# Performance work log

Hardware: AMD Instinct MI355X
Metric: run time of the kernel (lower is better)

## Reference

```python
import jax, jax.numpy as jnp
import numpy as np

N_NODES = 100000
N_EDGES = 1600000
HID = 64


def _gcn_conv(x, src, dst, W, b, n_nodes):
    """PyG GCNConv: add self-loops, symmetric deg normalization, linear transform.
    out_i = sum_{j in N(i) u {i}} deg_i^{-1/2} deg_j^{-1/2} (x_j W) + b
    """
    h = x @ W  # [N, out] small matmul
    loops = jnp.arange(n_nodes, dtype=src.dtype)
    s = jnp.concatenate([src, loops])  # sources (message senders)
    d = jnp.concatenate([dst, loops])  # targets (aggregation index)
    deg = jax.ops.segment_sum(jnp.ones_like(d, dtype=h.dtype), d, num_segments=n_nodes)
    dinv = jnp.where(deg > 0, jax.lax.rsqrt(deg), 0.0)
    coef = dinv[s] * dinv[d]  # [E+N]
    msg = h[s] * coef[:, None]  # gather + scale (memory-bound)
    out = jax.ops.segment_sum(msg, d, num_segments=n_nodes)  # scatter-add
    return out + b


def setup_inputs() -> dict:
    key = jax.random.key(0)
    ks = jax.random.split(key, 16)
    x = jax.random.normal(ks[0], (N_NODES, 4), dtype=jnp.float32)
    edge_index = jax.random.randint(ks[1], (2, N_EDGES), 0, N_NODES, dtype=jnp.int64)
    s = 0.1
    params = {
        'W1': jax.random.normal(ks[2], (4, HID), dtype=jnp.float32) * s,
        'b1': jnp.zeros((HID,), dtype=jnp.float32),
        'W2': jax.random.normal(ks[3], (HID, HID), dtype=jnp.float32) * s,
        'b2': jnp.zeros((HID,), dtype=jnp.float32),
        'W3': jax.random.normal(ks[4], (HID, HID), dtype=jnp.float32) * s,
        'b3': jnp.zeros((HID,), dtype=jnp.float32),
        'Wp': jax.random.normal(ks[5], (HID, HID), dtype=jnp.float32) * s,
        'bp': jnp.zeros((HID,), dtype=jnp.float32),
        'Wa': jax.random.normal(ks[6], (HID, 4), dtype=jnp.float32) * s,
        'ba': jnp.zeros((4,), dtype=jnp.float32),
        'Wm': jax.random.normal(ks[7], (HID, 2), dtype=jnp.float32) * s,
        'bm': jnp.zeros((2,), dtype=jnp.float32),
        'Wg': jax.random.normal(ks[8], (HID, 3), dtype=jnp.float32) * s,
        'bg': jnp.zeros((3,), dtype=jnp.float32),
        'Wt': jax.random.normal(ks[9], (HID, 10), dtype=jnp.float32) * s,
        'bt': jnp.zeros((10,), dtype=jnp.float32),
    }
    return {'x': x, 'edge_index': edge_index, 'node_index': 0, **params}


def reference(x, edge_index, node_index, W1, b1, W2, b2, W3, b3, Wp, bp, Wa, ba, Wm, bm, Wg, bg, Wt, bt):
    src, dst = edge_index[0], edge_index[1]
    n = x.shape[0]
    # dropout is identity in eval mode
    h = jax.nn.relu(_gcn_conv(x, src, dst, W1, b1, n))
    h = jax.nn.relu(_gcn_conv(h, src, dst, W2, b2, n))
    h = jax.nn.relu(_gcn_conv(h, src, dst, W3, b3, n))
    node = h[node_index]
    node = jax.nn.relu(node @ Wp + bp)
    return (node @ Wa + ba, node @ Wm + bm, node @ Wg + bg, node @ Wt + bt)
```

## Files before the change

kernel.cpp:

```cpp
#include <hip/hip_runtime.h>


#define HID  64
#define CAP1 2048
#define CAP2 512
#define RB1  128
#define RB2  128
#define CL3  2048
#define VE   8
#define TPB  256

__device__ __forceinline__ int detect64(const void* ei) {
  const unsigned* e32 = (const unsigned*)ei;
  int lane = threadIdx.x & 63;
  bool z = (e32[2 * lane + 1] == 0u);
  return (__ballot(z) == ~0ull) ? 1 : 0;
}

__device__ __forceinline__ int ld_src(const void* ei, int is64, long long e) {
  return is64 ? (int)((const unsigned*)ei)[e << 1] : ((const int*)ei)[e];
}

__device__ __forceinline__ int load_dsts(const void* ei, long long E, long long base,
                                         int is64, int d[VE]) {
  int n = (int)((E - base) < VE ? (E - base) : VE);
  if (is64) {
    const unsigned long long* p = (const unsigned long long*)ei + E + base;
    if (n == VE && (((E + base) & 1) == 0)) {
      const ulonglong2* q = (const ulonglong2*)p;
#pragma unroll
      for (int k = 0; k < VE / 2; ++k) {
        ulonglong2 v = q[k];
        d[2 * k] = (int)(unsigned)v.x; d[2 * k + 1] = (int)(unsigned)v.y;
      }
    } else {
      for (int k = 0; k < n; ++k) d[k] = (int)(unsigned)p[k];
    }
  } else {
    const int* p = (const int*)ei + E + base;
    if (n == VE && (((E + base) & 3) == 0)) {
      const int4* q = (const int4*)p;
#pragma unroll
      for (int k = 0; k < VE / 4; ++k) {
        int4 v = q[k];
        d[4 * k] = v.x; d[4 * k + 1] = v.y; d[4 * k + 2] = v.z; d[4 * k + 3] = v.w;
      }
    } else {
      for (int k = 0; k < n; ++k) d[k] = p[k];
    }
  }
  return n;
}

__device__ __forceinline__ int load_dsts32(const int* dst32, long long E,
                                           long long base, int d[VE]) {
  int n = (int)((E - base) < VE ? (E - base) : VE);
  if (n == VE) {
    int4 a = ((const int4*)(dst32 + base))[0];
    int4 b = ((const int4*)(dst32 + base))[1];
    d[0] = a.x; d[1] = a.y; d[2] = a.z; d[3] = a.w;
    d[4] = b.x; d[5] = b.y; d[6] = b.z; d[7] = b.w;
  } else {
    for (int k = 0; k < n; ++k) d[k] = dst32[base + k];
  }
  return n;
}

__global__ void k_scanF1(const void* ei, int E, const int* nidx_p, int* dst32,
                         int* slot2, int* node2, int* cnt2, int* l3, int* ec3) {
  int is64 = detect64(ei);
  int nidx = *nidx_p;
  if (blockIdx.x == 0 && threadIdx.x == 0) {
    if (atomicCAS(&slot2[nidx], -1, -2) == -1) {
      int p = atomicAdd(cnt2, 1) & (CAP2 - 1);
      slot2[nidx] = p; node2[p] = nidx;
    }
  }
  long long base = ((long long)blockIdx.x * TPB + threadIdx.x) * VE;
  if (base >= E) return;
  int d[VE];
  int n = load_dsts(ei, E, base, is64, d);
  if (n == VE) {
    ((int4*)(dst32 + base))[0] = make_int4(d[0], d[1], d[2], d[3]);
    ((int4*)(dst32 + base))[1] = make_int4(d[4], d[5], d[6], d[7]);
  } else {
    for (int k = 0; k < n; ++k) dst32[base + k] = d[k];
  }
  for (int k = 0; k < n; ++k) {
    if (d[k] == nidx) {
      int s = ld_src(ei, is64, base + k);
      if (atomicCAS(&slot2[s], -1, -2) == -1) {
        int p = atomicAdd(cnt2, 1) & (CAP2 - 1);
        slot2[s] = p; node2[p] = s;
      }
      int q = atomicAdd(ec3, 1);
      if (q < CL3) l3[q] = s;
    }
  }
}

__global__ void k_scanF2(const void* ei, int E, const int* dst32,
                         const int* slot2, const int* node2, const int* cnt2,
                         int* slot1, int* node1, int* need, int* cnt1,
                         int* rc2, int* bl2) {
  int rows2 = min(*cnt2, CAP2);
  for (int r = threadIdx.x; r < rows2; r += TPB) {
    int i = node2[r];
    need[i] = 1;
    if (atomicCAS(&slot1[i], -1, -2) == -1) {
      int p = atomicAdd(cnt1, 1) & (CAP1 - 1);
      slot1[i] = p; node1[p] = i;
    }
  }
  int is64 = detect64(ei);
  long long base = ((long long)blockIdx.x * TPB + threadIdx.x) * VE;
  if (base >= E) return;
  int d[VE];
  int n = load_dsts32(dst32, E, base, d);
  for (int k = 0; k < n; ++k) {
    int ad = slot2[d[k]];
    if (ad >= 0) {
      int s = ld_src(ei, is64, base + k);
      need[s] = 1;
      if (atomicCAS(&slot1[s], -1, -2) == -1) {
        int p = atomicAdd(cnt1, 1) & (CAP1 - 1);
        slot1[s] = p; node1[p] = s;
      }
      int q = atomicAdd(&rc2[ad], 1);
      if (q < RB2) bl2[ad * RB2 + q] = s;
    }
  }
}

__global__ void k_scanS(const void* ei, int E, const int* dst32,
                        const int* slot1, int* need, int* rc1, int* bl1) {
  int is64 = detect64(ei);
  long long base = ((long long)blockIdx.x * TPB + threadIdx.x) * VE;
  if (base >= E) return;
  int d[VE];
  int n = load_dsts32(dst32, E, base, d);
  for (int k = 0; k < n; ++k) {
    int ad = slot1[d[k]];
    if (ad >= 0) {
      int s = ld_src(ei, is64, base + k);
      need[s] = 1;
      int q = atomicAdd(&rc1[ad], 1);
      if (q < RB1) bl1[ad * RB1 + q] = s;
    }
  }
}

__global__ void k_scanDeg(int E, const int* dst32, const int* need, int* deg) {
  long long base = ((long long)blockIdx.x * TPB + threadIdx.x) * VE;
  if (base >= E) return;
  int d[VE];
  int n = load_dsts32(dst32, E, base, d);
  for (int k = 0; k < n; ++k)
    if (need[d[k]]) atomicAdd(&deg[d[k]], 1);
}

__global__ void k_l1(const float* __restrict__ x, const float* __restrict__ W1,
                     const float* __restrict__ b1, const int* __restrict__ deg,
                     const int* __restrict__ node1, const int* __restrict__ cnt1,
                     const int* __restrict__ rc1, const int* __restrict__ bl1,
                     float* __restrict__ h1c) {
  int w = blockIdx.x * 4 + (threadIdx.x >> 6);
  int lane = threadIdx.x & 63;
  int rows = min(*cnt1, CAP1);
  if (w >= rows) return;
  int i = node1[w];
  float di = 1.0f / sqrtf((float)(deg[i] + 1));
  int cnt = min(rc1[w], RB1);
  float ax = 0.f, ay = 0.f, az = 0.f, aw = 0.f;
  for (int j = lane; j < cnt; j += 64) {
    int s = bl1[w * RB1 + j];
    float c = (1.0f / sqrtf((float)(deg[s] + 1))) * di;
    float4 xv = ((const float4*)x)[s];
    ax += c * xv.x; ay += c * xv.y; az += c * xv.z; aw += c * xv.w;
  }
#pragma unroll
  for (int t = 1; t < 64; t <<= 1) {
    ax += __shfl_xor(ax, t); ay += __shfl_xor(ay, t);
    az += __shfl_xor(az, t); aw += __shfl_xor(aw, t);
  }
  float4 xi = ((const float4*)x)[i];
  float dd = di * di;
  ax += dd * xi.x; ay += dd * xi.y; az += dd * xi.z; aw += dd * xi.w;
  float v = ax * W1[lane] + ay * W1[64 + lane] + az * W1[128 + lane] +
            aw * W1[192 + lane] + b1[lane];
  h1c[w * HID + lane] = v > 0.f ? v : 0.f;
}

__global__ __launch_bounds__(TPB) void k_l2tail(
    const float* W2, const float* b2, const int* deg,
    const int* node2, const int* cnt2, const int* slot1,
    const int* rc2, const int* bl2, const float* h1c, float* h2c,
    const int* nidx_p, const int* slot2, const int* l3, const int* ec3,
    const float* W3, const float* b3, const float* Wp, const float* bp,
    const float* Wa, const float* ba, const float* Wm, const float* bm,
    const float* Wg, const float* bg, const float* Wt, const float* bt,
    float* out) {
  __shared__ float h2s[64][HID];
  __shared__ float smA[4][HID];
  __shared__ float g3[HID];
  __shared__ float h3v[HID];
  __shared__ float pj[HID];
  __shared__ int   ssl[64];
  __shared__ float scc[64];
  int tid = threadIdx.x, wv = tid >> 6, lane = tid & 63;
  int nidx = *nidx_p;
  int rows = min(*cnt2, CAP2);

  for (int w = wv; w < rows; w += 4) {
    int i = node2[w];
    float di = 1.0f / sqrtf((float)(deg[i] + 1));
    int cnt = min(rc2[w], RB2);
    float acc = 0.f;
    for (int j0 = 0; j0 < cnt; j0 += 64) {
      int nb = min(64, cnt - j0);
      int sl = 0; float c = 0.f;
      if (lane < nb) {
        int s = bl2[w * RB2 + j0 + lane];
        sl = slot1[s];
        c = (1.0f / sqrtf((float)(deg[s] + 1))) * di;
      }
      for (int j = 0; j < nb; ++j)
        acc += __shfl(c, j) * h1c[__shfl(sl, j) * HID + lane];
    }
    acc += di * di * h1c[slot1[i] * HID + lane];
    smA[wv][lane] = acc;
    float v = b2[lane];
#pragma unroll 16
    for (int k = 0; k < HID; ++k) v += smA[wv][k] * W2[k * HID + lane];
    v = v > 0.f ? v : 0.f;
    if (w < 64) h2s[w][lane] = v; else h2c[w * HID + lane] = v;
  }
  __syncthreads();

  float dn = 1.0f / sqrtf((float)(deg[nidx] + 1));
  int cnt = min(*ec3, CL3);
  float acc = 0.f;
  for (int j0 = 0; j0 < cnt; j0 += 64) {
    int nb = min(64, cnt - j0);
    if (tid < nb) {
      int s = l3[j0 + tid];
      ssl[tid] = slot2[s];
      scc[tid] = (1.0f / sqrtf((float)(deg[s] + 1))) * dn;
    }
    __syncthreads();
    for (int j = wv; j < nb; j += 4) {
      int r = ssl[j];
      float hv = (r < 64) ? h2s[r][lane] : h2c[r * HID + lane];
      acc += scc[j] * hv;
    }
    __syncthreads();
  }
  smA[wv][lane] = acc;
  __syncthreads();
  if (wv == 0) {
    int r = slot2[nidx];
    float hv = (r < 64) ? h2s[r][lane] : h2c[r * HID + lane];
    g3[lane] = smA[0][lane] + smA[1][lane] + smA[2][lane] + smA[3][lane] +
               dn * dn * hv;
  }
  __syncthreads();
  if (wv == 0) {
    float v = b3[lane];
#pragma unroll 16
    for (int k = 0; k < HID; ++k) v += g3[k] * W3[k * HID + lane];
    h3v[lane] = v > 0.f ? v : 0.f;
  }
  __syncthreads();
  if (wv == 0) {
    float v = bp[lane];
#pragma unroll 16
    for (int k = 0; k < HID; ++k) v += h3v[k] * Wp[k * HID + lane];
    pj[lane] = v > 0.f ? v : 0.f;
  }
  __syncthreads();
  if (tid < 4) {
    float o = ba[tid];
    for (int k = 0; k < HID; ++k) o += pj[k] * Wa[k * 4 + tid];
    out[tid] = o;
  } else if (tid < 6) {
    int c = tid - 4; float o = bm[c];
    for (int k = 0; k < HID; ++k) o += pj[k] * Wm[k * 2 + c];
    out[tid] = o;
  } else if (tid < 9) {
    int c = tid - 6; float o = bg[c];
    for (int k = 0; k < HID; ++k) o += pj[k] * Wg[k * 3 + c];
    out[tid] = o;
  } else if (tid < 19) {
    int c = tid - 9; float o = bt[c];
    for (int k = 0; k < HID; ++k) o += pj[k] * Wt[k * 10 + c];
    out[tid] = o;
  }
}

extern "C" void kernel_launch(void* const* d_in, const int* in_sizes, int n_in,
                              void* d_out, int out_size, void* d_ws, size_t ws_size,
                              hipStream_t stream) {
  const float* x  = (const float*)d_in[0];
  const void*  ei = d_in[1];
  const int* nidx = (const int*)d_in[2];
  const float* W1 = (const float*)d_in[3];
  const float* b1 = (const float*)d_in[4];
  const float* W2 = (const float*)d_in[5];
  const float* b2 = (const float*)d_in[6];
  const float* W3 = (const float*)d_in[7];
  const float* b3 = (const float*)d_in[8];
  const float* Wp = (const float*)d_in[9];
  const float* bp = (const float*)d_in[10];
  const float* Wa = (const float*)d_in[11];
  const float* ba = (const float*)d_in[12];
  const float* Wm = (const float*)d_in[13];
  const float* bm = (const float*)d_in[14];
  const float* Wg = (const float*)d_in[15];
  const float* bg = (const float*)d_in[16];
  const float* Wt = (const float*)d_in[17];
  const float* bt = (const float*)d_in[18];
  float* out = (float*)d_out;

  int N = in_sizes[0] / 4;
  int E = in_sizes[1] / 2;

  char* w = (char*)d_ws;
  size_t o = 0;
  auto take = [&](size_t bytes) -> void* {
    void* p = w + o;
    o += (bytes + 255) & ~(size_t)255;
    return p;
  };
  size_t zeroBytes = (size_t)(3 + 2 * N + CAP1 + CAP2) * 4;
  int* zr = (int*)take(zeroBytes);
  int* cnt1 = zr + 0;
  int* cnt2 = zr + 1;
  int* ec3  = zr + 2;
  int* deg  = zr + 3;
  int* need = deg + N;
  int* rc1  = need + N;
  int* rc2  = rc1 + CAP1;
  int* slots = (int*)take((size_t)2 * N * 4);
  int* slot1 = slots;
  int* slot2 = slots + N;
  int*   dst32 = (int*)take((size_t)E * 4);
  int*   node1 = (int*)take((size_t)CAP1 * 4);
  int*   node2 = (int*)take((size_t)CAP2 * 4);
  int*   bl1   = (int*)take((size_t)CAP1 * RB1 * 4);
  int*   bl2   = (int*)take((size_t)CAP2 * RB2 * 4);
  int*   l3    = (int*)take((size_t)CL3 * 4);
  float* h1c   = (float*)take((size_t)CAP1 * HID * 4);
  float* h2c   = (float*)take((size_t)CAP2 * HID * 4);

  int gS = (int)(((long long)E + TPB * VE - 1) / (TPB * VE));

  hipMemsetAsync(zr, 0x00, zeroBytes, stream);
  hipMemsetAsync(slots, 0xFF, (size_t)2 * N * 4, stream);
  k_scanF1 <<<gS, TPB, 0, stream>>>(ei, E, nidx, dst32, slot2, node2, cnt2, l3, ec3);
  k_scanF2 <<<gS, TPB, 0, stream>>>(ei, E, dst32, slot2, node2, cnt2,
                                    slot1, node1, need, cnt1, rc2, bl2);
  k_scanS  <<<gS, TPB, 0, stream>>>(ei, E, dst32, slot1, need, rc1, bl1);
  k_scanDeg<<<gS, TPB, 0, stream>>>(E, dst32, need, deg);
  k_l1     <<<CAP1 / 4, TPB, 0, stream>>>(x, W1, b1, deg, node1, cnt1, rc1, bl1, h1c);
  k_l2tail <<<1, TPB, 0, stream>>>(W2, b2, deg, node2, cnt2, slot1, rc2, bl2,
                                   h1c, h2c, nidx, slot2, l3, ec3, W3, b3,
                                   Wp, bp, Wa, ba, Wm, bm, Wg, bg, Wt, bt, out);
}
```

Measured before the change: 194.3 us.

## Split layer-2 aggregation out of single-block tail into a multi-block kernel

Layer-2 row computation previously ran inside a single 256-thread block, with four waves looping over up to 512 rows. It now runs as its own kernel with CAP2/4 blocks, one wave per row, and the tail kernel reads all h2 rows from global memory instead of partly from shared memory. This spreads the layer-2 gather and matvec across many CUs, at the cost of one extra kernel launch and the loss of the shared-memory cache for the first 64 rows.

```diff
diff --git a/kernel.cpp b/kernel.cpp
--- a/kernel.cpp
+++ b/kernel.cpp
@@ -191,52 +191,58 @@
   h1c[w * HID + lane] = v > 0.f ? v : 0.f;
 }
 
-__global__ __launch_bounds__(TPB) void k_l2tail(
-    const float* W2, const float* b2, const int* deg,
-    const int* node2, const int* cnt2, const int* slot1,
-    const int* rc2, const int* bl2, const float* h1c, float* h2c,
-    const int* nidx_p, const int* slot2, const int* l3, const int* ec3,
-    const float* W3, const float* b3, const float* Wp, const float* bp,
-    const float* Wa, const float* ba, const float* Wm, const float* bm,
-    const float* Wg, const float* bg, const float* Wt, const float* bt,
-    float* out) {
-  __shared__ float h2s[64][HID];
-  __shared__ float smA[4][HID];
+__global__ void k_l2(const float* __restrict__ W2, const float* __restrict__ b2,
+                     const int* __restrict__ deg, const int* __restrict__ node2,
+                     const int* __restrict__ cnt2, const int* __restrict__ slot1,
+                     const int* __restrict__ rc2, const int* __restrict__ bl2,
+                     const float* __restrict__ h1c, float* __restrict__ h2c) {
+  __shared__ float sh[4][HID];
+  int wv = threadIdx.x >> 6, lane = threadIdx.x & 63;
+  int w = blockIdx.x * 4 + wv;
+  int rows = min(*cnt2, CAP2);
+  if (w >= rows) return;
+  int i = node2[w];
+  float di = 1.0f / sqrtf((float)(deg[i] + 1));
+  int cnt = min(rc2[w], RB2);
+  float acc = 0.f;
+  for (int j0 = 0; j0 < cnt; j0 += 64) {
+    int nb = min(64, cnt - j0);
+    int sl = 0; float c = 0.f;
+    if (lane < nb) {
+      int s = bl2[w * RB2 + j0 + lane];
+      sl = slot1[s];
+      c = (1.0f / sqrtf((float)(deg[s] + 1))) * di;
+    }
+    for (int j = 0; j < nb; ++j) {
+      int slj = __shfl(sl, j);
+      float cj = __shfl(c, j);
+      acc += cj * h1c[slj * HID + lane];
+    }
+  }
+  acc += di * di * h1c[slot1[i] * HID + lane];
+  sh[wv][lane] = acc;
+  float v = b2[lane];
+#pragma unroll 16
+  for (int k = 0; k < HID; ++k) v += sh[wv][k] * W2[k * HID + lane];
+  h2c[w * HID + lane] = v > 0.f ? v : 0.f;
+}
+
+__global__ void k_tail(const int* nidx_p, const int* slot2, const int* deg,
+                       const float* h2c, const int* l3, const int* ec3,
+                       const float* W3, const float* b3,
+                       const float* Wp, const float* bp,
+                       const float* Wa, const float* ba,
+                       const float* Wm, const float* bm,
+                       const float* Wg, const float* bg,
+                       const float* Wt, const float* bt, float* out) {
+  __shared__ float part[4][HID];
   __shared__ float g3[HID];
-  __shared__ float h3v[HID];
-  __shared__ float pj[HID];
+  __shared__ float h3[HID];
+  __shared__ float p[HID];
   __shared__ int   ssl[64];
   __shared__ float scc[64];
   int tid = threadIdx.x, wv = tid >> 6, lane = tid & 63;
   int nidx = *nidx_p;
-  int rows = min(*cnt2, CAP2);
-
-  for (int w = wv; w < rows; w += 4) {
-    int i = node2[w];
-    float di = 1.0f / sqrtf((float)(deg[i] + 1));
-    int cnt = min(rc2[w], RB2);
-    float acc = 0.f;
-    for (int j0 = 0; j0 < cnt; j0 += 64) {
-      int nb = min(64, cnt - j0);
-      int sl = 0; float c = 0.f;
-      if (lane < nb) {
-        int s = bl2[w * RB2 + j0 + lane];
-        sl = slot1[s];
-        c = (1.0f / sqrtf((float)(deg[s] + 1))) * di;
-      }
-      for (int j = 0; j < nb; ++j)
-        acc += __shfl(c, j) * h1c[__shfl(sl, j) * HID + lane];
-    }
-    acc += di * di * h1c[slot1[i] * HID + lane];
-    smA[wv][lane] = acc;
-    float v = b2[lane];
-#pragma unroll 16
-    for (int k = 0; k < HID; ++k) v += smA[wv][k] * W2[k * HID + lane];
-    v = v > 0.f ? v : 0.f;
-    if (w < 64) h2s[w][lane] = v; else h2c[w * HID + lane] = v;
-  }
-  __syncthreads();
-
   float dn = 1.0f / sqrtf((float)(deg[nidx] + 1));
   int cnt = min(*ec3, CL3);
   float acc = 0.f;
@@ -248,51 +254,47 @@
       scc[tid] = (1.0f / sqrtf((float)(deg[s] + 1))) * dn;
     }
     __syncthreads();
-    for (int j = wv; j < nb; j += 4) {
-      int r = ssl[j];
-      float hv = (r < 64) ? h2s[r][lane] : h2c[r * HID + lane];
-      acc += scc[j] * hv;
-    }
+    for (int j = wv; j < nb; j += 4)
+      acc += scc[j] * h2c[ssl[j] * HID + lane];
     __syncthreads();
   }
-  smA[wv][lane] = acc;
+  part[wv][lane] = acc;
   __syncthreads();
   if (wv == 0) {
-    int r = slot2[nidx];
-    float hv = (r < 64) ? h2s[r][lane] : h2c[r * HID + lane];
-    g3[lane] = smA[0][lane] + smA[1][lane] + smA[2][lane] + smA[3][lane] +
-               dn * dn * hv;
+    float a = part[0][lane] + part[1][lane] + part[2][lane] + part[3][lane];
+    a += dn * dn * h2c[slot2[nidx] * HID + lane];
+    g3[lane] = a;
   }
   __syncthreads();
   if (wv == 0) {
     float v = b3[lane];
 #pragma unroll 16
     for (int k = 0; k < HID; ++k) v += g3[k] * W3[k * HID + lane];
-    h3v[lane] = v > 0.f ? v : 0.f;
+    h3[lane] = v > 0.f ? v : 0.f;
   }
   __syncthreads();
   if (wv == 0) {
-    float v = bp[lane];
+    float pv = bp[lane];
 #pragma unroll 16
-    for (int k = 0; k < HID; ++k) v += h3v[k] * Wp[k * HID + lane];
-    pj[lane] = v > 0.f ? v : 0.f;
+    for (int k = 0; k < HID; ++k) pv += h3[k] * Wp[k * HID + lane];
+    p[lane] = pv > 0.f ? pv : 0.f;
   }
   __syncthreads();
   if (tid < 4) {
     float o = ba[tid];
-    for (int k = 0; k < HID; ++k) o += pj[k] * Wa[k * 4 + tid];
+    for (int k = 0; k < HID; ++k) o += p[k] * Wa[k * 4 + tid];
     out[tid] = o;
   } else if (tid < 6) {
     int c = tid - 4; float o = bm[c];
-    for (int k = 0; k < HID; ++k) o += pj[k] * Wm[k * 2 + c];
+    for (int k = 0; k < HID; ++k) o += p[k] * Wm[k * 2 + c];
     out[tid] = o;
   } else if (tid < 9) {
     int c = tid - 6; float o = bg[c];
-    for (int k = 0; k < HID; ++k) o += pj[k] * Wg[k * 3 + c];
+    for (int k = 0; k < HID; ++k) o += p[k] * Wg[k * 3 + c];
     out[tid] = o;
   } else if (tid < 19) {
     int c = tid - 9; float o = bt[c];
-    for (int k = 0; k < HID; ++k) o += pj[k] * Wt[k * 10 + c];
+    for (int k = 0; k < HID; ++k) o += p[k] * Wt[k * 10 + c];
     out[tid] = o;
   }
 }
@@ -362,7 +364,7 @@
   k_scanS  <<<gS, TPB, 0, stream>>>(ei, E, dst32, slot1, need, rc1, bl1);
   k_scanDeg<<<gS, TPB, 0, stream>>>(E, dst32, need, deg);
   k_l1     <<<CAP1 / 4, TPB, 0, stream>>>(x, W1, b1, deg, node1, cnt1, rc1, bl1, h1c);
-  k_l2tail <<<1, TPB, 0, stream>>>(W2, b2, deg, node2, cnt2, slot1, rc2, bl2,
-                                   h1c, h2c, nidx, slot2, l3, ec3, W3, b3,
-                                   Wp, bp, Wa, ba, Wm, bm, Wg, bg, Wt, bt, out);
-}
+  k_l2     <<<CAP2 / 4, TPB, 0, stream>>>(W2, b2, deg, node2, cnt2, slot1, rc2, bl2, h1c, h2c);
+  k_tail   <<<1, TPB, 0, stream>>>(nidx, slot2, deg, h2c, l3, ec3, W3, b3, Wp, bp,
+                                   Wa, ba, Wm, bm, Wg, bg, Wt, bt, out);
+}
```

Result: faster. 172.6 us (-11.2%).

## Fuse degree scan, layer 1, layer 2 and tail into one persistent kernel

Applied to the files above, without the earlier changes.

Merges the degree-count scan, the layer-1 kernel, and the layer-2 plus tail kernel into one grid of 256 blocks. The stages are separated by atomic ticket counters with spin-waits, and late-arriving blocks carry on to the next stage while the others exit. Slot arrays now use 0 as the empty marker with values offset by one, so a single zeroing memset replaces the separate 0xFF memset. This removes kernel launch gaps and one memset, but relies on the waiting blocks being co-resident. It also drops the shared-memory cache of layer-2 rows and uses a fixed grid-stride for the degree scan.

```diff
diff --git a/kernel.cpp b/kernel.cpp
--- a/kernel.cpp
+++ b/kernel.cpp
@@ -9,6 +9,9 @@
 #define CL3  2048
 #define VE   8
 #define TPB  256
+#define GC   256
+#define NL1  128
+#define NL2  8
 
 __device__ __forceinline__ int detect64(const void* ei) {
   const unsigned* e32 = (const unsigned*)ei;
@@ -66,14 +69,15 @@
   return n;
 }
 
+
 __global__ void k_scanF1(const void* ei, int E, const int* nidx_p, int* dst32,
                          int* slot2, int* node2, int* cnt2, int* l3, int* ec3) {
   int is64 = detect64(ei);
   int nidx = *nidx_p;
   if (blockIdx.x == 0 && threadIdx.x == 0) {
-    if (atomicCAS(&slot2[nidx], -1, -2) == -1) {
+    if (atomicCAS(&slot2[nidx], 0, -1) == 0) {
       int p = atomicAdd(cnt2, 1) & (CAP2 - 1);
-      slot2[nidx] = p; node2[p] = nidx;
+      slot2[nidx] = p + 1; node2[p] = nidx;
     }
   }
   long long base = ((long long)blockIdx.x * TPB + threadIdx.x) * VE;
@@ -89,9 +93,9 @@
   for (int k = 0; k < n; ++k) {
     if (d[k] == nidx) {
       int s = ld_src(ei, is64, base + k);
-      if (atomicCAS(&slot2[s], -1, -2) == -1) {
+      if (atomicCAS(&slot2[s], 0, -1) == 0) {
         int p = atomicAdd(cnt2, 1) & (CAP2 - 1);
-        slot2[s] = p; node2[p] = s;
+        slot2[s] = p + 1; node2[p] = s;
       }
       int q = atomicAdd(ec3, 1);
       if (q < CL3) l3[q] = s;
@@ -107,9 +111,9 @@
   for (int r = threadIdx.x; r < rows2; r += TPB) {
     int i = node2[r];
     need[i] = 1;
-    if (atomicCAS(&slot1[i], -1, -2) == -1) {
+    if (atomicCAS(&slot1[i], 0, -1) == 0) {
       int p = atomicAdd(cnt1, 1) & (CAP1 - 1);
-      slot1[i] = p; node1[p] = i;
+      slot1[i] = p + 1; node1[p] = i;
     }
   }
   int is64 = detect64(ei);
@@ -118,13 +122,14 @@
   int d[VE];
   int n = load_dsts32(dst32, E, base, d);
   for (int k = 0; k < n; ++k) {
-    int ad = slot2[d[k]];
-    if (ad >= 0) {
+    int sv = slot2[d[k]];
+    if (sv > 0) {
+      int ad = sv - 1;
       int s = ld_src(ei, is64, base + k);
       need[s] = 1;
-      if (atomicCAS(&slot1[s], -1, -2) == -1) {
+      if (atomicCAS(&slot1[s], 0, -1) == 0) {
         int p = atomicAdd(cnt1, 1) & (CAP1 - 1);
-        slot1[s] = p; node1[p] = s;
+        slot1[s] = p + 1; node1[p] = s;
       }
       int q = atomicAdd(&rc2[ad], 1);
       if (q < RB2) bl2[ad * RB2 + q] = s;
@@ -140,8 +145,9 @@
   int d[VE];
   int n = load_dsts32(dst32, E, base, d);
   for (int k = 0; k < n; ++k) {
-    int ad = slot1[d[k]];
-    if (ad >= 0) {
+    int sv = slot1[d[k]];
+    if (sv > 0) {
+      int ad = sv - 1;
       int s = ld_src(ei, is64, base + k);
       need[s] = 1;
       int q = atomicAdd(&rc1[ad], 1);
@@ -150,150 +156,198 @@
   }
 }
 
-__global__ void k_scanDeg(int E, const int* dst32, const int* need, int* deg) {
-  long long base = ((long long)blockIdx.x * TPB + threadIdx.x) * VE;
-  if (base >= E) return;
-  int d[VE];
-  int n = load_dsts32(dst32, E, base, d);
-  for (int k = 0; k < n; ++k)
-    if (need[d[k]]) atomicAdd(&deg[d[k]], 1);
-}
-
-__global__ void k_l1(const float* __restrict__ x, const float* __restrict__ W1,
-                     const float* __restrict__ b1, const int* __restrict__ deg,
-                     const int* __restrict__ node1, const int* __restrict__ cnt1,
-                     const int* __restrict__ rc1, const int* __restrict__ bl1,
-                     float* __restrict__ h1c) {
-  int w = blockIdx.x * 4 + (threadIdx.x >> 6);
-  int lane = threadIdx.x & 63;
-  int rows = min(*cnt1, CAP1);
-  if (w >= rows) return;
-  int i = node1[w];
-  float di = 1.0f / sqrtf((float)(deg[i] + 1));
-  int cnt = min(rc1[w], RB1);
-  float ax = 0.f, ay = 0.f, az = 0.f, aw = 0.f;
-  for (int j = lane; j < cnt; j += 64) {
-    int s = bl1[w * RB1 + j];
-    float c = (1.0f / sqrtf((float)(deg[s] + 1))) * di;
-    float4 xv = ((const float4*)x)[s];
-    ax += c * xv.x; ay += c * xv.y; az += c * xv.z; aw += c * xv.w;
-  }
-#pragma unroll
-  for (int t = 1; t < 64; t <<= 1) {
-    ax += __shfl_xor(ax, t); ay += __shfl_xor(ay, t);
-    az += __shfl_xor(az, t); aw += __shfl_xor(aw, t);
-  }
-  float4 xi = ((const float4*)x)[i];
-  float dd = di * di;
-  ax += dd * xi.x; ay += dd * xi.y; az += dd * xi.z; aw += dd * xi.w;
-  float v = ax * W1[lane] + ay * W1[64 + lane] + az * W1[128 + lane] +
-            aw * W1[192 + lane] + b1[lane];
-  h1c[w * HID + lane] = v > 0.f ? v : 0.f;
-}
-
-__global__ __launch_bounds__(TPB) void k_l2tail(
-    const float* W2, const float* b2, const int* deg,
-    const int* node2, const int* cnt2, const int* slot1,
-    const int* rc2, const int* bl2, const float* h1c, float* h2c,
-    const int* nidx_p, const int* slot2, const int* l3, const int* ec3,
-    const float* W3, const float* b3, const float* Wp, const float* bp,
-    const float* Wa, const float* ba, const float* Wm, const float* bm,
-    const float* Wg, const float* bg, const float* Wt, const float* bt,
-    float* out) {
-  __shared__ float h2s[64][HID];
-  __shared__ float smA[4][HID];
+__global__ __launch_bounds__(TPB) void k_compute(
+    int E, const int* __restrict__ dst32, const int* __restrict__ need,
+    int* __restrict__ deg,
+    const float* __restrict__ x, const float* __restrict__ W1,
+    const float* __restrict__ b1, const int* __restrict__ node1,
+    const int* __restrict__ cnt1, const int* __restrict__ rc1,
+    const int* __restrict__ bl1, float* __restrict__ h1c,
+    const float* __restrict__ W2, const float* __restrict__ b2,
+    const int* __restrict__ node2, const int* __restrict__ cnt2,
+    const int* __restrict__ slot1, const int* __restrict__ rc2,
+    const int* __restrict__ bl2, float* __restrict__ h2c,
+    const int* __restrict__ nidx_p, const int* __restrict__ slot2,
+    const int* __restrict__ l3, const int* __restrict__ ec3,
+    const float* __restrict__ W3, const float* __restrict__ b3,
+    const float* __restrict__ Wp, const float* __restrict__ bp,
+    const float* __restrict__ Wa, const float* __restrict__ ba,
+    const float* __restrict__ Wm, const float* __restrict__ bm,
+    const float* __restrict__ Wg, const float* __restrict__ bg,
+    const float* __restrict__ Wt, const float* __restrict__ bt,
+    float* __restrict__ out,
+    int* tickD, int* tickL1, int* tickL2) {
+  const int tid = threadIdx.x;
+  const int lane = tid & 63, wv = tid >> 6;
+  __shared__ int s_t;
+  __shared__ float sh[4][HID];
   __shared__ float g3[HID];
   __shared__ float h3v[HID];
   __shared__ float pj[HID];
   __shared__ int   ssl[64];
   __shared__ float scc[64];
-  int tid = threadIdx.x, wv = tid >> 6, lane = tid & 63;
-  int nidx = *nidx_p;
-  int rows = min(*cnt2, CAP2);
-
-  for (int w = wv; w < rows; w += 4) {
-    int i = node2[w];
-    float di = 1.0f / sqrtf((float)(deg[i] + 1));
-    int cnt = min(rc2[w], RB2);
+
+  for (long long base = ((long long)blockIdx.x * TPB + tid) * VE;
+       base < E; base += (long long)GC * TPB * VE) {
+    int d[VE]; int n = load_dsts32(dst32, E, base, d);
+    for (int k = 0; k < n; ++k)
+      if (need[d[k]]) atomicAdd(&deg[d[k]], 1);
+  }
+  __syncthreads();
+  if (tid == 0) {
+    __threadfence();
+    s_t = __hip_atomic_fetch_add(tickD, 1, __ATOMIC_ACQ_REL,
+                                 __HIP_MEMORY_SCOPE_AGENT);
+  }
+  __syncthreads();
+  int t = s_t;
+  if (t < GC - NL1) return;
+  if (tid == 0) {
+    while (__hip_atomic_load(tickD, __ATOMIC_ACQUIRE,
+                             __HIP_MEMORY_SCOPE_AGENT) < GC)
+      __builtin_amdgcn_s_sleep(2);
+  }
+  __syncthreads();
+
+  {
+    int r1 = t - (GC - NL1);
+    int rows1 = min(*cnt1, CAP1);
+    for (int w = r1 * 4 + wv; w < rows1; w += NL1 * 4) {
+      int i = node1[w];
+      float di = 1.0f / sqrtf((float)(deg[i] + 1));
+      int cnt = min(rc1[w], RB1);
+      float ax = 0.f, ay = 0.f, az = 0.f, aw = 0.f;
+      for (int j = lane; j < cnt; j += 64) {
+        int s = bl1[w * RB1 + j];
+        float c = (1.0f / sqrtf((float)(deg[s] + 1))) * di;
+        float4 xv = ((const float4*)x)[s];
+        ax += c * xv.x; ay += c * xv.y; az += c * xv.z; aw += c * xv.w;
+      }
+#pragma unroll
+      for (int u = 1; u < 64; u <<= 1) {
+        ax += __shfl_xor(ax, u); ay += __shfl_xor(ay, u);
+        az += __shfl_xor(az, u); aw += __shfl_xor(aw, u);
+      }
+      float4 xi = ((const float4*)x)[i];
+      float dd = di * di;
+      ax += dd * xi.x; ay += dd * xi.y; az += dd * xi.z; aw += dd * xi.w;
+      float v = ax * W1[lane] + ay * W1[64 + lane] + az * W1[128 + lane] +
+                aw * W1[192 + lane] + b1[lane];
+      h1c[w * HID + lane] = v > 0.f ? v : 0.f;
+    }
+  }
+  __syncthreads();
+  if (tid == 0) {
+    __threadfence();
+    s_t = __hip_atomic_fetch_add(tickL1, 1, __ATOMIC_ACQ_REL,
+                                 __HIP_MEMORY_SCOPE_AGENT);
+  }
+  __syncthreads();
+  t = s_t;
+  if (t < NL1 - NL2) return;
+  if (tid == 0) {
+    while (__hip_atomic_load(tickL1, __ATOMIC_ACQUIRE,
+                             __HIP_MEMORY_SCOPE_AGENT) < NL1)
+      __builtin_amdgcn_s_sleep(2);
+  }
+  __syncthreads();
+
+  int rows2 = min(*cnt2, CAP2);
+  {
+    int r2 = t - (NL1 - NL2);
+    for (int w = r2 * 4 + wv; w < rows2; w += NL2 * 4) {
+      int i = node2[w];
+      float di = 1.0f / sqrtf((float)(deg[i] + 1));
+      int cnt = min(rc2[w], RB2);
+      float acc = 0.f;
+      for (int j0 = 0; j0 < cnt; j0 += 64) {
+        int nb = min(64, cnt - j0);
+        int sl = 0; float c = 0.f;
+        if (lane < nb) {
+          int s = bl2[w * RB2 + j0 + lane];
+          sl = slot1[s] - 1;
+          c = (1.0f / sqrtf((float)(deg[s] + 1))) * di;
+        }
+        for (int j = 0; j < nb; ++j) {
+          int slj = __shfl(sl, j);
+          float cj = __shfl(c, j);
+          acc += cj * h1c[slj * HID + lane];
+        }
+      }
+      acc += di * di * h1c[(slot1[i] - 1) * HID + lane];
+      sh[wv][lane] = acc;
+      float v = b2[lane];
+#pragma unroll 16
+      for (int k = 0; k < HID; ++k) v += sh[wv][k] * W2[k * HID + lane];
+      h2c[w * HID + lane] = v > 0.f ? v : 0.f;
+    }
+  }
+  __syncthreads();
+  if (tid == 0) {
+    __threadfence();
+    s_t = __hip_atomic_fetch_add(tickL2, 1, __ATOMIC_ACQ_REL,
+                                 __HIP_MEMORY_SCOPE_AGENT);
+  }
+  __syncthreads();
+  t = s_t;
+  if (t != NL2 - 1) return;
+
+  {
+    int nidx = *nidx_p;
+    float dn = 1.0f / sqrtf((float)(deg[nidx] + 1));
+    int cnt = min(*ec3, CL3);
     float acc = 0.f;
     for (int j0 = 0; j0 < cnt; j0 += 64) {
       int nb = min(64, cnt - j0);
-      int sl = 0; float c = 0.f;
-      if (lane < nb) {
-        int s = bl2[w * RB2 + j0 + lane];
-        sl = slot1[s];
-        c = (1.0f / sqrtf((float)(deg[s] + 1))) * di;
-      }
-      for (int j = 0; j < nb; ++j)
-        acc += __shfl(c, j) * h1c[__shfl(sl, j) * HID + lane];
-    }
-    acc += di * di * h1c[slot1[i] * HID + lane];
-    smA[wv][lane] = acc;
-    float v = b2[lane];
+      if (tid < nb) {
+        int s = l3[j0 + tid];
+        ssl[tid] = slot2[s] - 1;
+        scc[tid] = (1.0f / sqrtf((float)(deg[s] + 1))) * dn;
+      }
+      __syncthreads();
+      for (int j = wv; j < nb; j += 4)
+        acc += scc[j] * h2c[ssl[j] * HID + lane];
+      __syncthreads();
+    }
+    sh[wv][lane] = acc;
+    __syncthreads();
+    if (wv == 0) {
+      float a = sh[0][lane] + sh[1][lane] + sh[2][lane] + sh[3][lane];
+      a += dn * dn * h2c[(slot2[nidx] - 1) * HID + lane];
+      g3[lane] = a;
+    }
+    __syncthreads();
+    if (wv == 0) {
+      float v = b3[lane];
 #pragma unroll 16
-    for (int k = 0; k < HID; ++k) v += smA[wv][k] * W2[k * HID + lane];
-    v = v > 0.f ? v : 0.f;
-    if (w < 64) h2s[w][lane] = v; else h2c[w * HID + lane] = v;
-  }
-  __syncthreads();
-
-  float dn = 1.0f / sqrtf((float)(deg[nidx] + 1));
-  int cnt = min(*ec3, CL3);
-  float acc = 0.f;
-  for (int j0 = 0; j0 < cnt; j0 += 64) {
-    int nb = min(64, cnt - j0);
-    if (tid < nb) {
-      int s = l3[j0 + tid];
-      ssl[tid] = slot2[s];
-      scc[tid] = (1.0f / sqrtf((float)(deg[s] + 1))) * dn;
+      for (int k = 0; k < HID; ++k) v += g3[k] * W3[k * HID + lane];
+      h3v[lane] = v > 0.f ? v : 0.f;
     }
     __syncthreads();
-    for (int j = wv; j < nb; j += 4) {
-      int r = ssl[j];
-      float hv = (r < 64) ? h2s[r][lane] : h2c[r * HID + lane];
-      acc += scc[j] * hv;
+    if (wv == 0) {
+      float v = bp[lane];
+#pragma unroll 16
+      for (int k = 0; k < HID; ++k) v += h3v[k] * Wp[k * HID + lane];
+      pj[lane] = v > 0.f ? v : 0.f;
     }
     __syncthreads();
-  }
-  smA[wv][lane] = acc;
-  __syncthreads();
-  if (wv == 0) {
-    int r = slot2[nidx];
-    float hv = (r < 64) ? h2s[r][lane] : h2c[r * HID + lane];
-    g3[lane] = smA[0][lane] + smA[1][lane] + smA[2][lane] + smA[3][lane] +
-               dn * dn * hv;
-  }
-  __syncthreads();
-  if (wv == 0) {
-    float v = b3[lane];
-#pragma unroll 16
-    for (int k = 0; k < HID; ++k) v += g3[k] * W3[k * HID + lane];
-    h3v[lane] = v > 0.f ? v : 0.f;
-  }
-  __syncthreads();
-  if (wv == 0) {
-    float v = bp[lane];
-#pragma unroll 16
-    for (int k = 0; k < HID; ++k) v += h3v[k] * Wp[k * HID + lane];
-    pj[lane] = v > 0.f ? v : 0.f;
-  }
-  __syncthreads();
-  if (tid < 4) {
-    float o = ba[tid];
-    for (int k = 0; k < HID; ++k) o += pj[k] * Wa[k * 4 + tid];
-    out[tid] = o;
-  } else if (tid < 6) {
-    int c = tid - 4; float o = bm[c];
-    for (int k = 0; k < HID; ++k) o += pj[k] * Wm[k * 2 + c];
-    out[tid] = o;
-  } else if (tid < 9) {
-    int c = tid - 6; float o = bg[c];
-    for (int k = 0; k < HID; ++k) o += pj[k] * Wg[k * 3 + c];
-    out[tid] = o;
-  } else if (tid < 19) {
-    int c = tid - 9; float o = bt[c];
-    for (int k = 0; k < HID; ++k) o += pj[k] * Wt[k * 10 + c];
-    out[tid] = o;
+    if (tid < 4) {
+      float o = ba[tid];
+      for (int k = 0; k < HID; ++k) o += pj[k] * Wa[k * 4 + tid];
+      out[tid] = o;
+    } else if (tid < 6) {
+      int c = tid - 4; float o = bm[c];
+      for (int k = 0; k < HID; ++k) o += pj[k] * Wm[k * 2 + c];
+      out[tid] = o;
+    } else if (tid < 9) {
+      int c = tid - 6; float o = bg[c];
+      for (int k = 0; k < HID; ++k) o += pj[k] * Wg[k * 3 + c];
+      out[tid] = o;
+    } else if (tid < 19) {
+      int c = tid - 9; float o = bt[c];
+      for (int k = 0; k < HID; ++k) o += pj[k] * Wt[k * 10 + c];
+      out[tid] = o;
+    }
   }
 }
 
@@ -331,18 +385,20 @@
     o += (bytes + 255) & ~(size_t)255;
     return p;
   };
-  size_t zeroBytes = (size_t)(3 + 2 * N + CAP1 + CAP2) * 4;
-  int* zr = (int*)take(zeroBytes);
-  int* cnt1 = zr + 0;
-  int* cnt2 = zr + 1;
-  int* ec3  = zr + 2;
-  int* deg  = zr + 3;
-  int* need = deg + N;
-  int* rc1  = need + N;
-  int* rc2  = rc1 + CAP1;
-  int* slots = (int*)take((size_t)2 * N * 4);
-  int* slot1 = slots;
-  int* slot2 = slots + N;
+  size_t zeroInts = (size_t)(8 + 2 * N + CAP1 + CAP2) + (size_t)2 * N;
+  int* zr = (int*)take(zeroInts * 4);
+  int* cnt1  = zr + 0;
+  int* cnt2  = zr + 1;
+  int* ec3   = zr + 2;
+  int* tickD = zr + 3;
+  int* tickL1= zr + 4;
+  int* tickL2= zr + 5;
+  int* deg   = zr + 8;
+  int* need  = deg + N;
+  int* rc1   = need + N;
+  int* rc2   = rc1 + CAP1;
+  int* slot1 = rc2 + CAP2;
+  int* slot2 = slot1 + N;
   int*   dst32 = (int*)take((size_t)E * 4);
   int*   node1 = (int*)take((size_t)CAP1 * 4);
   int*   node2 = (int*)take((size_t)CAP2 * 4);
@@ -354,15 +410,15 @@
 
   int gS = (int)(((long long)E + TPB * VE - 1) / (TPB * VE));
 
-  hipMemsetAsync(zr, 0x00, zeroBytes, stream);
-  hipMemsetAsync(slots, 0xFF, (size_t)2 * N * 4, stream);
+  hipMemsetAsync(zr, 0x00, zeroInts * 4, stream);
   k_scanF1 <<<gS, TPB, 0, stream>>>(ei, E, nidx, dst32, slot2, node2, cnt2, l3, ec3);
   k_scanF2 <<<gS, TPB, 0, stream>>>(ei, E, dst32, slot2, node2, cnt2,
                                     slot1, node1, need, cnt1, rc2, bl2);
   k_scanS  <<<gS, TPB, 0, stream>>>(ei, E, dst32, slot1, need, rc1, bl1);
-  k_scanDeg<<<gS, TPB, 0, stream>>>(E, dst32, need, deg);
-  k_l1     <<<CAP1 / 4, TPB, 0, stream>>>(x, W1, b1, deg, node1, cnt1, rc1, bl1, h1c);
-  k_l2tail <<<1, TPB, 0, stream>>>(W2, b2, deg, node2, cnt2, slot1, rc2, bl2,
-                                   h1c, h2c, nidx, slot2, l3, ec3, W3, b3,
-                                   Wp, bp, Wa, ba, Wm, bm, Wg, bg, Wt, bt, out);
-}
+  k_compute<<<GC, TPB, 0, stream>>>(E, dst32, need, deg,
+                                    x, W1, b1, node1, cnt1, rc1, bl1, h1c,
+                                    W2, b2, node2, cnt2, slot1, rc2, bl2, h2c,
+                                    nidx, slot2, l3, ec3, W3, b3, Wp, bp,
+                                    Wa, ba, Wm, bm, Wg, bg, Wt, bt, out,
+                                    tickD, tickL1, tickL2);
+}
```

Result: slower. 199.6 us (+2.7%).
